# Optimization experiments

Measured on AMD Instinct MI355X. Metric: run time of the kernel, lower is better.

Reference implementation:

```python
import jax, jax.numpy as jnp
import numpy as np

N, D_IN, D_H, D_OUT, E = 32768, 1024, 2048, 1024, 8

def setup_inputs() -> dict:
    key = jax.random.key(0)
    ks = jax.random.split(key, 8)
    s_in = 1.0 / np.sqrt(D_IN)
    s_h = 1.0 / np.sqrt(D_H)
    return {
        "x": jax.random.normal(ks[0], (N, D_IN), dtype=jnp.float32),
        "Wr": jax.random.normal(ks[1], (D_IN, E), dtype=jnp.float32) * s_in,
        "br": jnp.zeros((E,), dtype=jnp.float32),
        "W1": jax.random.normal(ks[2], (E, D_IN, D_H), dtype=jnp.float32) * s_in,
        "b1": jnp.zeros((E, D_H), dtype=jnp.float32),
        "W2": jax.random.normal(ks[3], (E, D_H, D_OUT), dtype=jnp.float32) * s_h,
        "b2": jnp.zeros((E, D_OUT), dtype=jnp.float32),
    }

def reference(x, Wr, br, W1, b1, W2, b2):
    # Supervised router: encoder is Identity, router is Linear + softmax.
    router_probs = jax.nn.softmax(x @ Wr + br, axis=-1)            # [N, E]
    router_probs_max = jnp.max(router_probs, axis=-1)              # [N]
    routes = jnp.argmax(router_probs, axis=-1)                     # [N] int
    counts = jnp.sum(jax.nn.one_hot(routes, E, dtype=x.dtype), axis=0)  # [E]

    # Top-1 dispatch: each token goes through exactly one expert MLP.
    # Small fixed loop over experts (E=8); mask-combine replaces gather/scatter.
    out = jnp.zeros((N, D_OUT), dtype=x.dtype)
    for e in range(E):
        h = jax.nn.relu(x @ W1[e] + b1[e])                         # [N, D_H]
        y = h @ W2[e] + b2[e]                                      # [N, D_OUT]
        out = out + jnp.where((routes == e)[:, None], y, jnp.zeros((), x.dtype))
    # Straight-through scaling: value 1 in fwd, routes grad through router prob.
    scale = router_probs_max / jax.lax.stop_gradient(router_probs_max)
    out = out * scale[:, None]
    return out, router_probs, counts
```

## Files before the change

kernel.cpp:

```cpp
#include <hip/hip_runtime.h>
#include <stdint.h>


#define NTOK   32768
#define DIN    1024
#define DH     2048
#define DOUT   1024
#define NEXP   8

typedef unsigned short u16;
typedef __bf16 bf16x8 __attribute__((ext_vector_type(8)));
typedef float  f32x4  __attribute__((ext_vector_type(4)));
typedef unsigned short us8 __attribute__((ext_vector_type(8)));
typedef const __attribute__((address_space(1))) void gvoid_t;
typedef __attribute__((address_space(3))) void svoid_t;

__device__ __forceinline__ u16 f2bf(float f) {
  union { float f; uint32_t u; } v; v.f = f;
  return (u16)((v.u + 0x7FFFu + ((v.u >> 16) & 1u)) >> 16);
}

__global__ __launch_bounds__(256) void k_router(
    const float* __restrict__ x, const float* __restrict__ Wr,
    const float* __restrict__ br, float* __restrict__ probs,
    int* __restrict__ routes, u16* __restrict__ xb)
{
  __shared__ float wr_s[NEXP * DIN];
  int tid = threadIdx.x;
  for (int idx = tid; idx < DIN * NEXP / 4; idx += 256) {
    float4 v = ((const float4*)Wr)[idx];
    int k = idx >> 1, r = (idx & 1) * 4;
    wr_s[(r + 0) * DIN + k] = v.x;
    wr_s[(r + 1) * DIN + k] = v.y;
    wr_s[(r + 2) * DIN + k] = v.z;
    wr_s[(r + 3) * DIN + k] = v.w;
  }
  __syncthreads();
  int lane = tid & 63, wv = tid >> 6;
  int t = blockIdx.x * 4 + wv;
  const float* xr = x + (size_t)t * DIN;
  u16* xbrow = xb + (size_t)t * DIN;
  float acc[NEXP];
  #pragma unroll
  for (int e = 0; e < NEXP; ++e) acc[e] = 0.f;
  #pragma unroll
  for (int i = 0; i < 4; ++i) {
    int k = i * 256 + lane * 4;
    float4 xv = *(const float4*)(xr + k);
    ushort4 o;
    o.x = f2bf(xv.x); o.y = f2bf(xv.y); o.z = f2bf(xv.z); o.w = f2bf(xv.w);
    *(ushort4*)(xbrow + k) = o;
    #pragma unroll
    for (int e = 0; e < NEXP; ++e) {
      float4 w4 = *(const float4*)(wr_s + e * DIN + k);
      acc[e] += xv.x * w4.x + xv.y * w4.y + xv.z * w4.z + xv.w * w4.w;
    }
  }
  #pragma unroll
  for (int off = 32; off >= 1; off >>= 1) {
    #pragma unroll
    for (int e = 0; e < NEXP; ++e) acc[e] += __shfl_xor(acc[e], off, 64);
  }
  if (lane == 0) {
    float l[NEXP], m = -1e30f;
    #pragma unroll
    for (int e = 0; e < NEXP; ++e) { l[e] = acc[e] + br[e]; m = fmaxf(m, l[e]); }
    float p[NEXP], s = 0.f;
    #pragma unroll
    for (int e = 0; e < NEXP; ++e) { p[e] = expf(l[e] - m); s += p[e]; }
    float inv = 1.f / s;
    int am = 0; float best = l[0];
    #pragma unroll
    for (int e = 1; e < NEXP; ++e) if (l[e] > best) { best = l[e]; am = e; }
    float4 pa = {p[0] * inv, p[1] * inv, p[2] * inv, p[3] * inv};
    float4 pb = {p[4] * inv, p[5] * inv, p[6] * inv, p[7] * inv};
    float4* pd = (float4*)(probs + (size_t)t * NEXP);
    pd[0] = pa; pd[1] = pb;
    routes[t] = am;
  }
}

__global__ __launch_bounds__(256) void k_count(
    const int* __restrict__ routes, int* __restrict__ aux)
{
  int t = blockIdx.x * 256 + threadIdx.x;
  int e = routes[t];
  int lane = threadIdx.x & 63;
  #pragma unroll
  for (int ee = 0; ee < NEXP; ++ee) {
    unsigned long long m = __ballot(e == ee);
    if (lane == 0 && m) atomicAdd(&aux[ee], (int)__popcll(m));
  }
}

__global__ __launch_bounds__(256) void k_prefix(int* __restrict__ aux, float* __restrict__ counts_out)
{
  __shared__ int s_off[NEXP], s_cnt[NEXP], s_tb[NEXP], s_nt;
  int tid = threadIdx.x;
  if (tid == 0) {
    int off = 0, tb = 0;
    for (int e = 0; e < NEXP; ++e) {
      int c = aux[e];
      counts_out[e] = (float)c;
      s_cnt[e] = c; s_off[e] = off; s_tb[e] = tb;
      aux[24 + e] = off;
      off += c; tb += (c + 127) >> 7;
    }
    s_nt = tb;
    aux[16] = tb;
  }
  __syncthreads();
  int nt = s_nt;
  for (int i = tid; i < nt; i += 256) {
    int e = 0;
    #pragma unroll
    for (int k = 1; k < NEXP; ++k) if (i >= s_tb[k]) e = k;
    int tt = i - s_tb[e];
    aux[128 + i] = e;
    aux[512 + i] = s_off[e] + tt * 128;
    aux[896 + i] = s_off[e] + s_cnt[e];
  }
}

__global__ __launch_bounds__(256) void k_assign(
    const int* __restrict__ routes, int* __restrict__ aux,
    int* __restrict__ tok_of_pos)
{
  int t = blockIdx.x * 256 + threadIdx.x;
  int e = routes[t];
  int lane = threadIdx.x & 63;
  int p = 0;
  #pragma unroll
  for (int ee = 0; ee < NEXP; ++ee) {
    unsigned long long m = __ballot(e == ee);
    int base = 0;
    if (lane == 0 && m) base = atomicAdd(&aux[8 + ee], (int)__popcll(m));
    base = __shfl(base, 0, 64);
    if (e == ee)
      p = aux[24 + ee] + base + (int)__popcll(m & ((1ull << lane) - 1ull));
  }
  tok_of_pos[p] = t;
}

__global__ __launch_bounds__(256) void k_transpose(
    const float* __restrict__ W1, u16* __restrict__ W1t,
    const float* __restrict__ W2, u16* __restrict__ W2t)
{
  int z = blockIdx.z;
  const float* src; u16* dst; int K, Nn, e;
  if (z < NEXP) { src = W1; dst = W1t; K = DIN; Nn = DH;   e = z; }
  else          { src = W2; dst = W2t; K = DH;  Nn = DOUT; e = z - NEXP; }
  int k0 = blockIdx.x * 64, n0 = blockIdx.y * 64;
  if (k0 >= K || n0 >= Nn) return;
  __shared__ float tile[64][65];
  const float* s = src + ((size_t)e * K + k0) * Nn + n0;
  int r = threadIdx.x >> 6, c = threadIdx.x & 63;
  #pragma unroll
  for (int i = 0; i < 16; ++i)
    tile[r + i * 4][c] = s[(size_t)(r + i * 4) * Nn + c];
  __syncthreads();
  u16* d = dst + ((size_t)e * Nn + n0) * K + k0;
  int kg = (threadIdx.x & 7) * 8, nr0 = threadIdx.x >> 3;
  #pragma unroll
  for (int p = 0; p < 2; ++p) {
    int nr = nr0 + p * 32;
    us8 o;
    #pragma unroll
    for (int j = 0; j < 8; ++j) o[j] = f2bf(tile[kg + j][nr]);
    *(us8*)(d + (size_t)nr * K + kg) = o;
  }
}

template<int MODE, int GATHER>
__global__ __launch_bounds__(256, 4) void k_gemm(
    const u16* __restrict__ A, const u16* __restrict__ Bt,
    const float* __restrict__ bias, u16* __restrict__ Hout,
    float* __restrict__ Yout, const int* __restrict__ tok_of_pos,
    const int* __restrict__ aux, int K, int Nn, int nbyl)
{
  int nwg = gridDim.x;
  int bid = blockIdx.x;
  int wg  = (bid & 7) * (nwg >> 3) + (bid >> 3);
  int by  = wg & ((1 << nbyl) - 1);
  int bx  = wg >> nbyl;
  if (bx >= aux[16]) return;
  int e  = aux[128 + bx];
  int r0 = aux[512 + bx];
  int r1 = aux[896 + bx];
  int bn0 = by << 7;

  __shared__ __align__(16) u16 As[128 * 64];
  __shared__ __align__(16) u16 Bs[128 * 64];

  int tid = threadIdx.x;
  int lane = tid & 63, wv = tid >> 6;
  int wr = wv >> 1, wc = wv & 1;
  const u16* Be = Bt + (size_t)e * Nn * K;

  int tk[4];
  #pragma unroll
  for (int r = 0; r < 4; ++r) {
    int gr = r0 + r * 32 + (tid >> 3);
    gr = gr < NTOK ? gr : NTOK - 1;
    tk[r] = GATHER ? tok_of_pos[gr] : gr;
  }

  auto stage = [&](int kt) {
    int k0 = kt * 64;
    #pragma unroll
    for (int r = 0; r < 4; ++r) {
      int L = (r * 256 + tid) * 16;
      int sl = ((L >> 4) & 7) ^ ((L >> 7) & 7);
      __builtin_amdgcn_global_load_lds(
          (gvoid_t*)((const char*)(A + (size_t)tk[r] * K + k0) + sl * 16),
          (svoid_t*)((char*)As + L), 16, 0, 0);
    }
    #pragma unroll
    for (int r = 0; r < 4; ++r) {
      int L = (r * 256 + tid) * 16;
      int row = L >> 7;
      int sl = ((L >> 4) & 7) ^ (row & 7);
      __builtin_amdgcn_global_load_lds(
          (gvoid_t*)((const char*)(Be + (size_t)(bn0 + row) * K + k0) + sl * 16),
          (svoid_t*)((char*)Bs + L), 16, 0, 0);
    }
  };

  f32x4 acc[4][4];
  #pragma unroll
  for (int i = 0; i < 4; ++i)
    #pragma unroll
    for (int j = 0; j < 4; ++j)
      acc[i][j] = (f32x4){0.f, 0.f, 0.f, 0.f};

  int KT = K >> 6;
  stage(0);
  for (int kt = 0; kt < KT; ++kt) {
    __syncthreads();
    const char* As_c = (const char*)As;
    const char* Bs_c = (const char*)Bs;
    #pragma unroll
    for (int kk = 0; kk < 2; ++kk) {
      int sw = ((kk * 4 + (lane >> 4)) ^ (lane & 7)) << 4;
      bf16x8 a[4], b[4];
      #pragma unroll
      for (int f = 0; f < 4; ++f)
        a[f] = *(const bf16x8*)(As_c + (wr * 64 + f * 16 + (lane & 15)) * 128 + sw);
      #pragma unroll
      for (int f = 0; f < 4; ++f)
        b[f] = *(const bf16x8*)(Bs_c + (wc * 64 + f * 16 + (lane & 15)) * 128 + sw);
      #pragma unroll
      for (int i = 0; i < 4; ++i)
        #pragma unroll
        for (int j = 0; j < 4; ++j)
          acc[i][j] = __builtin_amdgcn_mfma_f32_16x16x32_bf16(a[i], b[j], acc[i][j], 0, 0, 0);
    }
    __syncthreads();
    if (kt + 1 < KT) stage(kt + 1);
  }

  const float* be = bias + (size_t)e * Nn;
  float bv[4];
  #pragma unroll
  for (int j = 0; j < 4; ++j) bv[j] = be[bn0 + wc * 64 + j * 16 + (lane & 15)];
  #pragma unroll
  for (int i = 0; i < 4; ++i) {
    #pragma unroll
    for (int q = 0; q < 4; ++q) {
      int r = r0 + wr * 64 + i * 16 + (lane >> 4) * 4 + q;
      if (r < r1) {
        if (MODE == 0) {
          u16* dst = Hout + (size_t)r * Nn + bn0 + wc * 64 + (lane & 15);
          #pragma unroll
          for (int j = 0; j < 4; ++j)
            dst[j * 16] = f2bf(fmaxf(acc[i][j][q] + bv[j], 0.f));
        } else {
          int tok = tok_of_pos[r];
          float* dst = Yout + (size_t)tok * Nn + bn0 + wc * 64 + (lane & 15);
          #pragma unroll
          for (int j = 0; j < 4; ++j)
            dst[j * 16] = acc[i][j][q] + bv[j];
        }
      }
    }
  }
}

extern "C" void kernel_launch(void* const* d_in, const int* in_sizes, int n_in,
                              void* d_out, int out_size, void* d_ws, size_t ws_size,
                              hipStream_t stream)
{
  const float* x  = (const float*)d_in[0];
  const float* Wr = (const float*)d_in[1];
  const float* br = (const float*)d_in[2];
  const float* W1 = (const float*)d_in[3];
  const float* b1 = (const float*)d_in[4];
  const float* W2 = (const float*)d_in[5];
  const float* b2 = (const float*)d_in[6];

  float* out    = (float*)d_out;
  float* probs  = out + (size_t)NTOK * DOUT;
  float* counts = probs + (size_t)NTOK * NEXP;

  char* ws = (char*)d_ws;
  u16* xb          = (u16*)(ws);
  u16* h           = (u16*)(ws + 67108864);
  u16* W1t         = (u16*)(ws + 201326592);
  u16* W2t         = (u16*)(ws + 234881024);
  int* aux         = (int*)(ws + 268435456);
  int* routes      = (int*)(ws + 268451840);
  int* tok_of_pos  = (int*)(ws + 268582912);

  (void)hipMemsetAsync(aux, 0, 16384, stream);
  k_router<<<NTOK / 4, 256, 0, stream>>>(x, Wr, br, probs, routes, xb);
  k_count<<<NTOK / 256, 256, 0, stream>>>(routes, aux);
  k_transpose<<<dim3(32, 32, 2 * NEXP), 256, 0, stream>>>(W1, W1t, W2, W2t);
  k_prefix<<<1, 256, 0, stream>>>(aux, counts);
  k_assign<<<NTOK / 256, 256, 0, stream>>>(routes, aux, tok_of_pos);
  k_gemm<0, 1><<<264 * 16, 256, 0, stream>>>(xb, W1t, b1, h, nullptr, tok_of_pos, aux, DIN, DH, 4);
  k_gemm<1, 0><<<264 * 8, 256, 0, stream>>>(h, W2t, b2, nullptr, out, tok_of_pos, aux, DH, DOUT, 3);
}
```

Before: 526.6 us.

## Fuse expert counting into router and prefix into assign, amortize Wr loads

The router kernel now processes 16 tokens per wave, so the 32KB Wr shared-memory staging is amortized over 64 tokens per block, and it accumulates a per-block expert histogram flushed with atomics. This removes the separate count kernel. The prefix kernel is folded into the assign kernel: each block recomputes the expert offsets and block 0 writes the tile tables. Two kernel launches are dropped, at the cost of fewer router blocks and serial tile-table construction in one thread.

```diff
diff --git a/kernel.cpp b/kernel.cpp
--- a/kernel.cpp
+++ b/kernel.cpp
@@ -23,10 +23,12 @@
 __global__ __launch_bounds__(256) void k_router(
     const float* __restrict__ x, const float* __restrict__ Wr,
     const float* __restrict__ br, float* __restrict__ probs,
-    int* __restrict__ routes, u16* __restrict__ xb)
+    int* __restrict__ routes, u16* __restrict__ xb, int* __restrict__ aux)
 {
   __shared__ float wr_s[NEXP * DIN];
+  __shared__ int hist[NEXP];
   int tid = threadIdx.x;
+  if (tid < NEXP) hist[tid] = 0;
   for (int idx = tid; idx < DIN * NEXP / 4; idx += 256) {
     float4 v = ((const float4*)Wr)[idx];
     int k = idx >> 1, r = (idx & 1) * 4;
@@ -37,98 +39,86 @@
   }
   __syncthreads();
   int lane = tid & 63, wv = tid >> 6;
-  int t = blockIdx.x * 4 + wv;
-  const float* xr = x + (size_t)t * DIN;
-  u16* xbrow = xb + (size_t)t * DIN;
-  float acc[NEXP];
-  #pragma unroll
-  for (int e = 0; e < NEXP; ++e) acc[e] = 0.f;
-  #pragma unroll
-  for (int i = 0; i < 4; ++i) {
-    int k = i * 256 + lane * 4;
-    float4 xv = *(const float4*)(xr + k);
-    ushort4 o;
-    o.x = f2bf(xv.x); o.y = f2bf(xv.y); o.z = f2bf(xv.z); o.w = f2bf(xv.w);
-    *(ushort4*)(xbrow + k) = o;
-    #pragma unroll
-    for (int e = 0; e < NEXP; ++e) {
-      float4 w4 = *(const float4*)(wr_s + e * DIN + k);
-      acc[e] += xv.x * w4.x + xv.y * w4.y + xv.z * w4.z + xv.w * w4.w;
-    }
-  }
-  #pragma unroll
-  for (int off = 32; off >= 1; off >>= 1) {
-    #pragma unroll
-    for (int e = 0; e < NEXP; ++e) acc[e] += __shfl_xor(acc[e], off, 64);
-  }
-  if (lane == 0) {
-    float l[NEXP], m = -1e30f;
-    #pragma unroll
-    for (int e = 0; e < NEXP; ++e) { l[e] = acc[e] + br[e]; m = fmaxf(m, l[e]); }
-    float p[NEXP], s = 0.f;
-    #pragma unroll
-    for (int e = 0; e < NEXP; ++e) { p[e] = expf(l[e] - m); s += p[e]; }
-    float inv = 1.f / s;
-    int am = 0; float best = l[0];
-    #pragma unroll
-    for (int e = 1; e < NEXP; ++e) if (l[e] > best) { best = l[e]; am = e; }
-    float4 pa = {p[0] * inv, p[1] * inv, p[2] * inv, p[3] * inv};
-    float4 pb = {p[4] * inv, p[5] * inv, p[6] * inv, p[7] * inv};
-    float4* pd = (float4*)(probs + (size_t)t * NEXP);
-    pd[0] = pa; pd[1] = pb;
-    routes[t] = am;
-  }
-}
-
-__global__ __launch_bounds__(256) void k_count(
-    const int* __restrict__ routes, int* __restrict__ aux)
-{
-  int t = blockIdx.x * 256 + threadIdx.x;
-  int e = routes[t];
-  int lane = threadIdx.x & 63;
-  #pragma unroll
-  for (int ee = 0; ee < NEXP; ++ee) {
-    unsigned long long m = __ballot(e == ee);
-    if (lane == 0 && m) atomicAdd(&aux[ee], (int)__popcll(m));
-  }
-}
-
-__global__ __launch_bounds__(256) void k_prefix(int* __restrict__ aux, float* __restrict__ counts_out)
-{
-  __shared__ int s_off[NEXP], s_cnt[NEXP], s_tb[NEXP], s_nt;
+  int base = (blockIdx.x * 4 + wv) * 16;
+  for (int it = 0; it < 16; ++it) {
+    int t = base + it;
+    const float* xr = x + (size_t)t * DIN;
+    u16* xbrow = xb + (size_t)t * DIN;
+    float acc[NEXP];
+    #pragma unroll
+    for (int e = 0; e < NEXP; ++e) acc[e] = 0.f;
+    #pragma unroll
+    for (int i = 0; i < 4; ++i) {
+      int k = i * 256 + lane * 4;
+      float4 xv = *(const float4*)(xr + k);
+      ushort4 o;
+      o.x = f2bf(xv.x); o.y = f2bf(xv.y); o.z = f2bf(xv.z); o.w = f2bf(xv.w);
+      *(ushort4*)(xbrow + k) = o;
+      #pragma unroll
+      for (int e = 0; e < NEXP; ++e) {
+        float4 w4 = *(const float4*)(wr_s + e * DIN + k);
+        acc[e] += xv.x * w4.x + xv.y * w4.y + xv.z * w4.z + xv.w * w4.w;
+      }
+    }
+    #pragma unroll
+    for (int off = 32; off >= 1; off >>= 1) {
+      #pragma unroll
+      for (int e = 0; e < NEXP; ++e) acc[e] += __shfl_xor(acc[e], off, 64);
+    }
+    if (lane == 0) {
+      float l[NEXP], m = -1e30f;
+      #pragma unroll
+      for (int e = 0; e < NEXP; ++e) { l[e] = acc[e] + br[e]; m = fmaxf(m, l[e]); }
+      float p[NEXP], s = 0.f;
+      #pragma unroll
+      for (int e = 0; e < NEXP; ++e) { p[e] = expf(l[e] - m); s += p[e]; }
+      float inv = 1.f / s;
+      int am = 0; float best = l[0];
+      #pragma unroll
+      for (int e = 1; e < NEXP; ++e) if (l[e] > best) { best = l[e]; am = e; }
+      float4 pa = {p[0] * inv, p[1] * inv, p[2] * inv, p[3] * inv};
+      float4 pb = {p[4] * inv, p[5] * inv, p[6] * inv, p[7] * inv};
+      float4* pd = (float4*)(probs + (size_t)t * NEXP);
+      pd[0] = pa; pd[1] = pb;
+      routes[t] = am;
+      atomicAdd(&hist[am], 1);
+    }
+  }
+  __syncthreads();
+  if (tid < NEXP && hist[tid]) atomicAdd(&aux[tid], hist[tid]);
+}
+
+__global__ __launch_bounds__(256) void k_assign(
+    const int* __restrict__ routes, int* __restrict__ aux,
+    int* __restrict__ tok_of_pos, float* __restrict__ counts_out)
+{
+  __shared__ int s_off[NEXP];
   int tid = threadIdx.x;
-  if (tid == 0) {
+  if (tid < NEXP) {
+    int off = 0;
+    for (int k = 0; k < tid; ++k) off += aux[k];
+    s_off[tid] = off;
+  }
+  __syncthreads();
+  if (blockIdx.x == 0 && tid == 0) {
     int off = 0, tb = 0;
     for (int e = 0; e < NEXP; ++e) {
       int c = aux[e];
       counts_out[e] = (float)c;
-      s_cnt[e] = c; s_off[e] = off; s_tb[e] = tb;
-      aux[24 + e] = off;
-      off += c; tb += (c + 127) >> 7;
-    }
-    s_nt = tb;
+      int tiles = (c + 127) >> 7;
+      for (int tt = 0; tt < tiles; ++tt) {
+        aux[128 + tb] = e;
+        aux[512 + tb] = off + tt * 128;
+        aux[896 + tb] = off + c;
+        ++tb;
+      }
+      off += c;
+    }
     aux[16] = tb;
   }
-  __syncthreads();
-  int nt = s_nt;
-  for (int i = tid; i < nt; i += 256) {
-    int e = 0;
-    #pragma unroll
-    for (int k = 1; k < NEXP; ++k) if (i >= s_tb[k]) e = k;
-    int tt = i - s_tb[e];
-    aux[128 + i] = e;
-    aux[512 + i] = s_off[e] + tt * 128;
-    aux[896 + i] = s_off[e] + s_cnt[e];
-  }
-}
-
-__global__ __launch_bounds__(256) void k_assign(
-    const int* __restrict__ routes, int* __restrict__ aux,
-    int* __restrict__ tok_of_pos)
-{
-  int t = blockIdx.x * 256 + threadIdx.x;
+  int t = blockIdx.x * 256 + tid;
   int e = routes[t];
-  int lane = threadIdx.x & 63;
+  int lane = tid & 63;
   int p = 0;
   #pragma unroll
   for (int ee = 0; ee < NEXP; ++ee) {
@@ -137,7 +127,7 @@
     if (lane == 0 && m) base = atomicAdd(&aux[8 + ee], (int)__popcll(m));
     base = __shfl(base, 0, 64);
     if (e == ee)
-      p = aux[24 + ee] + base + (int)__popcll(m & ((1ull << lane) - 1ull));
+      p = s_off[ee] + base + (int)__popcll(m & ((1ull << lane) - 1ull));
   }
   tok_of_pos[p] = t;
 }
@@ -312,11 +302,9 @@
   int* tok_of_pos  = (int*)(ws + 268582912);
 
   (void)hipMemsetAsync(aux, 0, 16384, stream);
-  k_router<<<NTOK / 4, 256, 0, stream>>>(x, Wr, br, probs, routes, xb);
-  k_count<<<NTOK / 256, 256, 0, stream>>>(routes, aux);
+  k_router<<<NTOK / 64, 256, 0, stream>>>(x, Wr, br, probs, routes, xb, aux);
   k_transpose<<<dim3(32, 32, 2 * NEXP), 256, 0, stream>>>(W1, W1t, W2, W2t);
-  k_prefix<<<1, 256, 0, stream>>>(aux, counts);
-  k_assign<<<NTOK / 256, 256, 0, stream>>>(routes, aux, tok_of_pos);
+  k_assign<<<NTOK / 256, 256, 0, stream>>>(routes, aux, tok_of_pos, counts);
   k_gemm<0, 1><<<264 * 16, 256, 0, stream>>>(xb, W1t, b1, h, nullptr, tok_of_pos, aux, DIN, DH, 4);
   k_gemm<1, 0><<<264 * 8, 256, 0, stream>>>(h, W2t, b2, nullptr, out, tok_of_pos, aux, DH, DOUT, 3);
 }
```

Measured after the change: 473.2 us. 10.1% less time.
